# Performance work log

Measured on AMD Instinct MI355X. Metric: run time of the kernel, lower is better.

## Reference

```python
import jax, jax.numpy as jnp
from jax import lax
import numpy as np

K = 31      # avg_pool2d kernel_size
PAD = 15    # avg_pool2d padding
EPS = 1.0
GAMMA = 5.0


def _box_avg(x):
    # Separable 31x31 box filter, stride 1, zero padding 15,
    # count_include_pad=True (PyTorch default) -> always divide by K*K.
    s = lax.reduce_window(x, 0.0, lax.add, (1, 1, K, 1), (1, 1, 1, 1),
                          [(0, 0), (0, 0), (PAD, PAD), (0, 0)])
    s = lax.reduce_window(s, 0.0, lax.add, (1, 1, 1, K), (1, 1, 1, 1),
                          [(0, 0), (0, 0), (0, 0), (PAD, PAD)])
    return s / (K * K)


def setup_inputs() -> dict:
    key = jax.random.key(0)
    k1, k2 = jax.random.split(key)
    shape = (64, 1, 512, 512)  # [B, C, H, W]
    inp = jax.random.uniform(k1, shape, dtype=jnp.float32)
    tgt = jax.random.uniform(k2, shape, dtype=jnp.float32)
    return {"input": inp, "target": tgt}


def reference(input, target):
    weight = 1.0 + GAMMA * jnp.abs(_box_avg(target) - target)
    intersection = jnp.sum(input * target * weight)
    denom = jnp.sum(input * weight) + jnp.sum(target * weight)
    dice = (2.0 * intersection + EPS) / (denom + EPS)
    return 1.0 - dice
```

## Files before the change

kernel.cpp:

```cpp
#include <hip/hip_runtime.h>


#define BATCH 64
#define H     512
#define W     512
#define RBAND 32
#define SLOTS 62
#define NBLK  (BATCH * (H / RBAND))

typedef _Float16 half8 __attribute__((ext_vector_type(8)));

__global__ __launch_bounds__(256, 2) void fused_kernel(const float* __restrict__ tgt,
                                                       const float* __restrict__ inp,
                                                       float4* __restrict__ partials) {
    const int tid  = threadIdx.x;
    const int lane = tid & 63;
    const int wv   = tid >> 6;
    const int g    = blockIdx.x;
    const int blk  = ((g & 7) << 7) | (g >> 3);
    const int band = blk & 15;
    const int b    = blk >> 4;
    const int R0   = band * RBAND;
    const float* timg = tgt + (size_t)b * H * W;
    const float* iimg = inp + (size_t)b * H * W;

    __shared__ __align__(16) unsigned ring[SLOTS * 256];

    const int col0 = lane * 8;
    const int ofs  = lane * 4;

    const float mL1 = (lane >= 1) ? 1.f : 0.f;
    const float mR1 = (lane <= 62) ? 1.f : 0.f;
    const float mL2 = (lane >= 2) ? 1.f : 0.f;
    const float mR2 = (lane <= 61) ? 1.f : 0.f;

    #pragma unroll 2
    for (int k = 0; k < 16; ++k) {
        const int idx = 4 * k + wv;
        if (idx < SLOTS) {
            const int row = R0 - 15 + idx;
            float t[8];
            #pragma unroll
            for (int q = 0; q < 8; ++q) t[q] = 0.f;
            if (row >= 0 && row < H) {
                const float4 v0 = *(const float4*)(timg + (size_t)row * W + col0);
                const float4 v1 = *(const float4*)(timg + (size_t)row * W + col0 + 4);
                t[0] = v0.x; t[1] = v0.y; t[2] = v0.z; t[3] = v0.w;
                t[4] = v1.x; t[5] = v1.y; t[6] = v1.z; t[7] = v1.w;
            }
            const float p1 = t[0];
            const float p2 = p1 + t[1];
            const float p3 = p2 + t[2];
            const float p4 = p3 + t[3];
            const float p5 = p4 + t[4];
            const float p6 = p5 + t[5];
            const float p7 = p6 + t[6];
            const float s  = p7 + t[7];
            const float f1 = s - p1, f2 = s - p2, f3 = s - p3, f4 = s - p4;
            const float f5 = s - p5, f6 = s - p6, f7 = s - p7;

            const float sL1 = __shfl_up(s, 1, 64);
            const float sR1 = __shfl_down(s, 1, 64);
            const float g1 = __shfl_up(f1, 2, 64);
            const float g2 = __shfl_up(f2, 2, 64);
            const float g3 = __shfl_up(f3, 2, 64);
            const float g4 = __shfl_up(f4, 2, 64);
            const float g5 = __shfl_up(f5, 2, 64);
            const float g6 = __shfl_up(f6, 2, 64);
            const float g7 = __shfl_up(f7, 2, 64);
            const float q1 = __shfl_down(p1, 2, 64);
            const float q2 = __shfl_down(p2, 2, 64);
            const float q3 = __shfl_down(p3, 2, 64);
            const float q4 = __shfl_down(p4, 2, 64);
            const float q5 = __shfl_down(p5, 2, 64);
            const float q6 = __shfl_down(p6, 2, 64);
            const float q7 = __shfl_down(p7, 2, 64);

            const float S3 = fmaf(mL1, sL1, fmaf(mR1, sR1, s));
            half8 hv;
            hv[0] = (_Float16)fmaf(mL2, g1, S3);
            hv[1] = (_Float16)fmaf(mL2, g2, fmaf(mR2, q1, S3));
            hv[2] = (_Float16)fmaf(mL2, g3, fmaf(mR2, q2, S3));
            hv[3] = (_Float16)fmaf(mL2, g4, fmaf(mR2, q3, S3));
            hv[4] = (_Float16)fmaf(mL2, g5, fmaf(mR2, q4, S3));
            hv[5] = (_Float16)fmaf(mL2, g6, fmaf(mR2, q5, S3));
            hv[6] = (_Float16)fmaf(mL2, g7, fmaf(mR2, q6, S3));
            hv[7] = (_Float16)fmaf(mR2, q7, S3);
            *(half8*)&ring[idx * 256 + ofs] = hv;
        }
    }
    __syncthreads();

    const int base = 8 * wv;
    float box[8];
    #pragma unroll
    for (int q = 0; q < 8; ++q) box[q] = 0.f;
    #pragma unroll 4
    for (int jj = 0; jj < 31; ++jj) {
        const half8 c = *(const half8*)&ring[(base + jj) * 256 + ofs];
        #pragma unroll
        for (int q = 0; q < 8; ++q) box[q] += (float)c[q];
    }

    const float inv = 1.0f / 961.0f;
    float aI = 0.f, aA = 0.f, aB = 0.f;

    #pragma unroll
    for (int st = 0; st < 8; ++st) {
        const int h = R0 + base + st;

        if (st > 0) {
            const half8 a = *(const half8*)&ring[(base + st + 30) * 256 + ofs];
            const half8 s = *(const half8*)&ring[(base + st - 1) * 256 + ofs];
            #pragma unroll
            for (int q = 0; q < 8; ++q) box[q] += (float)a[q] - (float)s[q];
        }

        const float4 i0 = *(const float4*)(iimg + (size_t)h * W + col0);
        const float4 i1 = *(const float4*)(iimg + (size_t)h * W + col0 + 4);
        const float4 t0 = *(const float4*)(timg + (size_t)h * W + col0);
        const float4 t1 = *(const float4*)(timg + (size_t)h * W + col0 + 4);
        const float tv[8] = {t0.x, t0.y, t0.z, t0.w, t1.x, t1.y, t1.z, t1.w};
        const float iv[8] = {i0.x, i0.y, i0.z, i0.w, i1.x, i1.y, i1.z, i1.w};

        #pragma unroll
        for (int k = 0; k < 8; ++k) {
            const float wgt = fmaf(5.0f, fabsf(fmaf(box[k], inv, -tv[k])), 1.0f);
            const float tw  = tv[k] * wgt;
            aI = fmaf(iv[k], tw, aI);
            aA = fmaf(iv[k], wgt, aA);
            aB += tw;
        }
    }

    #pragma unroll
    for (int off = 32; off > 0; off >>= 1) {
        aI += __shfl_down(aI, off, 64);
        aA += __shfl_down(aA, off, 64);
        aB += __shfl_down(aB, off, 64);
    }
    __syncthreads();
    float* rf = (float*)ring;
    if (lane == 0) { rf[wv] = aI; rf[8 + wv] = aA; rf[16 + wv] = aB; }
    __syncthreads();
    if (tid == 0) {
        float4 o;
        o.x = rf[0] + rf[1] + rf[2] + rf[3];
        o.y = rf[8] + rf[9] + rf[10] + rf[11];
        o.z = rf[16] + rf[17] + rf[18] + rf[19];
        o.w = 0.f;
        partials[g] = o;
    }
}

__global__ __launch_bounds__(1024) void reduce_kernel(const float4* __restrict__ partials,
                                                      float* __restrict__ out) {
    const int tid = threadIdx.x;
    const float4 v = partials[tid];
    float aI = v.x, aA = v.y, aB = v.z;
    #pragma unroll
    for (int off = 32; off > 0; off >>= 1) {
        aI += __shfl_down(aI, off, 64);
        aA += __shfl_down(aA, off, 64);
        aB += __shfl_down(aB, off, 64);
    }
    __shared__ float s[3][16];
    const int wvx = tid >> 6, ln = tid & 63;
    if (ln == 0) { s[0][wvx] = aI; s[1][wvx] = aA; s[2][wvx] = aB; }
    __syncthreads();
    if (tid == 0) {
        float I = 0.f, A = 0.f, Bv = 0.f;
        #pragma unroll
        for (int k = 0; k < 16; ++k) { I += s[0][k]; A += s[1][k]; Bv += s[2][k]; }
        out[0] = 1.0f - (2.0f * I + 1.0f) / (A + Bv + 1.0f);
    }
}

extern "C" void kernel_launch(void* const* d_in, const int* in_sizes, int n_in,
                              void* d_out, int out_size, void* d_ws, size_t ws_size,
                              hipStream_t stream) {
    const float* inp = (const float*)d_in[0];
    const float* tgt = (const float*)d_in[1];
    float* out = (float*)d_out;

    float4* partials = (float4*)d_ws;

    fused_kernel<<<NBLK, 256, 0, stream>>>(tgt, inp, partials);
    reduce_kernel<<<1, 1024, 0, stream>>>(partials, out);
}
```

Baseline: 163.3 us.

## Split fused box filter into global fp16 row-sum pass and sliding column pass

Replaces the single fused kernel, which stored horizontal box sums in an LDS ring per 32-row band, with two kernels. The first writes fp16 horizontal 31-wide sums for every row to a global workspace buffer. The second slides a vertical window down 32-row bands per wave, reading those sums back from global memory, and accumulates the dice terms. This drops the large LDS footprint and the per-band halo recomputation. In exchange it adds a 32 MB fp16 write and read round trip through global memory, plus an extra kernel launch.

```diff
diff --git a/kernel.cpp b/kernel.cpp
--- a/kernel.cpp
+++ b/kernel.cpp
@@ -4,30 +4,21 @@
 #define BATCH 64
 #define H     512
 #define W     512
-#define RBAND 32
-#define SLOTS 62
-#define NBLK  (BATCH * (H / RBAND))
+#define NROWS (BATCH * H)
+#define K1_BLOCKS 2048
+#define K1_WAVES  (K1_BLOCKS * 4)
+#define RB    32
+#define K2_BLOCKS 1024
 
 typedef _Float16 half8 __attribute__((ext_vector_type(8)));
+typedef _Float16 half2v __attribute__((ext_vector_type(2)));
 
-__global__ __launch_bounds__(256, 2) void fused_kernel(const float* __restrict__ tgt,
-                                                       const float* __restrict__ inp,
-                                                       float4* __restrict__ partials) {
+__global__ __launch_bounds__(256) void hrow_kernel(const float* __restrict__ tgt,
+                                                   _Float16* __restrict__ hbuf) {
     const int tid  = threadIdx.x;
     const int lane = tid & 63;
-    const int wv   = tid >> 6;
-    const int g    = blockIdx.x;
-    const int blk  = ((g & 7) << 7) | (g >> 3);
-    const int band = blk & 15;
-    const int b    = blk >> 4;
-    const int R0   = band * RBAND;
-    const float* timg = tgt + (size_t)b * H * W;
-    const float* iimg = inp + (size_t)b * H * W;
-
-    __shared__ __align__(16) unsigned ring[SLOTS * 256];
-
+    const int wid  = blockIdx.x * 4 + (tid >> 6);
     const int col0 = lane * 8;
-    const int ofs  = lane * 4;
 
     const float mL1 = (lane >= 1) ? 1.f : 0.f;
     const float mR1 = (lane <= 62) ? 1.f : 0.f;
@@ -35,102 +26,108 @@
     const float mR2 = (lane <= 61) ? 1.f : 0.f;
 
     #pragma unroll 2
-    for (int k = 0; k < 16; ++k) {
-        const int idx = 4 * k + wv;
-        if (idx < SLOTS) {
-            const int row = R0 - 15 + idx;
-            float t[8];
-            #pragma unroll
-            for (int q = 0; q < 8; ++q) t[q] = 0.f;
-            if (row >= 0 && row < H) {
-                const float4 v0 = *(const float4*)(timg + (size_t)row * W + col0);
-                const float4 v1 = *(const float4*)(timg + (size_t)row * W + col0 + 4);
-                t[0] = v0.x; t[1] = v0.y; t[2] = v0.z; t[3] = v0.w;
-                t[4] = v1.x; t[5] = v1.y; t[6] = v1.z; t[7] = v1.w;
-            }
-            const float p1 = t[0];
-            const float p2 = p1 + t[1];
-            const float p3 = p2 + t[2];
-            const float p4 = p3 + t[3];
-            const float p5 = p4 + t[4];
-            const float p6 = p5 + t[5];
-            const float p7 = p6 + t[6];
-            const float s  = p7 + t[7];
-            const float f1 = s - p1, f2 = s - p2, f3 = s - p3, f4 = s - p4;
-            const float f5 = s - p5, f6 = s - p6, f7 = s - p7;
+    for (int k = 0; k < 4; ++k) {
+        const int r = wid + K1_WAVES * k;
+        const float* trow = tgt + (size_t)r * W;
+        const float4 v0 = *(const float4*)(trow + col0);
+        const float4 v1 = *(const float4*)(trow + col0 + 4);
 
-            const float sL1 = __shfl_up(s, 1, 64);
-            const float sR1 = __shfl_down(s, 1, 64);
-            const float g1 = __shfl_up(f1, 2, 64);
-            const float g2 = __shfl_up(f2, 2, 64);
-            const float g3 = __shfl_up(f3, 2, 64);
-            const float g4 = __shfl_up(f4, 2, 64);
-            const float g5 = __shfl_up(f5, 2, 64);
-            const float g6 = __shfl_up(f6, 2, 64);
-            const float g7 = __shfl_up(f7, 2, 64);
-            const float q1 = __shfl_down(p1, 2, 64);
-            const float q2 = __shfl_down(p2, 2, 64);
-            const float q3 = __shfl_down(p3, 2, 64);
-            const float q4 = __shfl_down(p4, 2, 64);
-            const float q5 = __shfl_down(p5, 2, 64);
-            const float q6 = __shfl_down(p6, 2, 64);
-            const float q7 = __shfl_down(p7, 2, 64);
+        const float p1 = v0.x;
+        const float p2 = p1 + v0.y;
+        const float p3 = p2 + v0.z;
+        const float p4 = p3 + v0.w;
+        const float p5 = p4 + v1.x;
+        const float p6 = p5 + v1.y;
+        const float p7 = p6 + v1.z;
+        const float s  = p7 + v1.w;
+        const float f1 = s - p1, f2 = s - p2, f3 = s - p3, f4 = s - p4;
+        const float f5 = s - p5, f6 = s - p6, f7 = s - p7;
 
-            const float S3 = fmaf(mL1, sL1, fmaf(mR1, sR1, s));
-            half8 hv;
-            hv[0] = (_Float16)fmaf(mL2, g1, S3);
-            hv[1] = (_Float16)fmaf(mL2, g2, fmaf(mR2, q1, S3));
-            hv[2] = (_Float16)fmaf(mL2, g3, fmaf(mR2, q2, S3));
-            hv[3] = (_Float16)fmaf(mL2, g4, fmaf(mR2, q3, S3));
-            hv[4] = (_Float16)fmaf(mL2, g5, fmaf(mR2, q4, S3));
-            hv[5] = (_Float16)fmaf(mL2, g6, fmaf(mR2, q5, S3));
-            hv[6] = (_Float16)fmaf(mL2, g7, fmaf(mR2, q6, S3));
-            hv[7] = (_Float16)fmaf(mR2, q7, S3);
-            *(half8*)&ring[idx * 256 + ofs] = hv;
-        }
+        const float sL1 = __shfl_up(s, 1, 64);
+        const float sR1 = __shfl_down(s, 1, 64);
+        const float g1 = __shfl_up(f1, 2, 64);
+        const float g2 = __shfl_up(f2, 2, 64);
+        const float g3 = __shfl_up(f3, 2, 64);
+        const float g4 = __shfl_up(f4, 2, 64);
+        const float g5 = __shfl_up(f5, 2, 64);
+        const float g6 = __shfl_up(f6, 2, 64);
+        const float g7 = __shfl_up(f7, 2, 64);
+        const float q1 = __shfl_down(p1, 2, 64);
+        const float q2 = __shfl_down(p2, 2, 64);
+        const float q3 = __shfl_down(p3, 2, 64);
+        const float q4 = __shfl_down(p4, 2, 64);
+        const float q5 = __shfl_down(p5, 2, 64);
+        const float q6 = __shfl_down(p6, 2, 64);
+        const float q7 = __shfl_down(p7, 2, 64);
+
+        const float S3 = fmaf(mL1, sL1, fmaf(mR1, sR1, s));
+        half8 hv;
+        hv[0] = (_Float16)fmaf(mL2, g1, S3);
+        hv[1] = (_Float16)fmaf(mL2, g2, fmaf(mR2, q1, S3));
+        hv[2] = (_Float16)fmaf(mL2, g3, fmaf(mR2, q2, S3));
+        hv[3] = (_Float16)fmaf(mL2, g4, fmaf(mR2, q3, S3));
+        hv[4] = (_Float16)fmaf(mL2, g5, fmaf(mR2, q4, S3));
+        hv[5] = (_Float16)fmaf(mL2, g6, fmaf(mR2, q5, S3));
+        hv[6] = (_Float16)fmaf(mL2, g7, fmaf(mR2, q6, S3));
+        hv[7] = (_Float16)fmaf(mR2, q7, S3);
+        *(half8*)(hbuf + (size_t)r * W + col0) = hv;
     }
-    __syncthreads();
+}
 
-    const int base = 8 * wv;
-    float box[8];
-    #pragma unroll
-    for (int q = 0; q < 8; ++q) box[q] = 0.f;
-    #pragma unroll 4
-    for (int jj = 0; jj < 31; ++jj) {
-        const half8 c = *(const half8*)&ring[(base + jj) * 256 + ofs];
-        #pragma unroll
-        for (int q = 0; q < 8; ++q) box[q] += (float)c[q];
+__global__ __launch_bounds__(256) void main_kernel(const float* __restrict__ tgt,
+                                                   const float* __restrict__ inp,
+                                                   const _Float16* __restrict__ hbuf,
+                                                   float4* __restrict__ partials) {
+    const int tid  = threadIdx.x;
+    const int lane = tid & 63;
+    const int wv   = tid >> 6;
+    const int wid  = blockIdx.x * 4 + wv;
+    const int b     = wid >> 6;
+    const int inner = wid & 63;
+    const int cb    = inner & 3;
+    const int band  = inner >> 2;
+    const int r0    = band * RB;
+    const int col   = cb * 128 + lane * 2;
+
+    const float*    timg = tgt  + (size_t)b * H * W;
+    const float*    iimg = inp  + (size_t)b * H * W;
+    const _Float16* himg = hbuf + (size_t)b * H * W;
+
+    float box0 = 0.f, box1 = 0.f;
+    const int j0 = (r0 == 0) ? 15 : 0;
+    #pragma unroll 8
+    for (int j = j0; j < 31; ++j) {
+        const int row = r0 - 15 + j;
+        const half2v hv = *(const half2v*)(himg + (size_t)row * W + col);
+        box0 += (float)hv[0]; box1 += (float)hv[1];
     }
 
     const float inv = 1.0f / 961.0f;
     float aI = 0.f, aA = 0.f, aB = 0.f;
 
-    #pragma unroll
-    for (int st = 0; st < 8; ++st) {
-        const int h = R0 + base + st;
-
+    #pragma unroll 4
+    for (int st = 0; st < RB; ++st) {
+        const int h = r0 + st;
         if (st > 0) {
-            const half8 a = *(const half8*)&ring[(base + st + 30) * 256 + ofs];
-            const half8 s = *(const half8*)&ring[(base + st - 1) * 256 + ofs];
-            #pragma unroll
-            for (int q = 0; q < 8; ++q) box[q] += (float)a[q] - (float)s[q];
+            const int ra = h + 15;
+            const int rs = h - 16;
+            if (ra < H) {
+                const half2v hv = *(const half2v*)(himg + (size_t)ra * W + col);
+                box0 += (float)hv[0]; box1 += (float)hv[1];
+            }
+            if (rs >= 0) {
+                const half2v hv = *(const half2v*)(himg + (size_t)rs * W + col);
+                box0 -= (float)hv[0]; box1 -= (float)hv[1];
+            }
         }
-
-        const float4 i0 = *(const float4*)(iimg + (size_t)h * W + col0);
-        const float4 i1 = *(const float4*)(iimg + (size_t)h * W + col0 + 4);
-        const float4 t0 = *(const float4*)(timg + (size_t)h * W + col0);
-        const float4 t1 = *(const float4*)(timg + (size_t)h * W + col0 + 4);
-        const float tv[8] = {t0.x, t0.y, t0.z, t0.w, t1.x, t1.y, t1.z, t1.w};
-        const float iv[8] = {i0.x, i0.y, i0.z, i0.w, i1.x, i1.y, i1.z, i1.w};
-
-        #pragma unroll
-        for (int k = 0; k < 8; ++k) {
-            const float wgt = fmaf(5.0f, fabsf(fmaf(box[k], inv, -tv[k])), 1.0f);
-            const float tw  = tv[k] * wgt;
-            aI = fmaf(iv[k], tw, aI);
-            aA = fmaf(iv[k], wgt, aA);
-            aB += tw;
-        }
+        const float2 tv = *(const float2*)(timg + (size_t)h * W + col);
+        const float2 iv = *(const float2*)(iimg + (size_t)h * W + col);
+        const float w0 = fmaf(5.0f, fabsf(fmaf(box0, inv, -tv.x)), 1.0f);
+        const float w1 = fmaf(5.0f, fabsf(fmaf(box1, inv, -tv.y)), 1.0f);
+        const float tw0 = tv.x * w0, tw1 = tv.y * w1;
+        aI = fmaf(iv.x, tw0, fmaf(iv.y, tw1, aI));
+        aA = fmaf(iv.x, w0,  fmaf(iv.y, w1,  aA));
+        aB += tw0 + tw1;
     }
 
     #pragma unroll
@@ -139,17 +136,16 @@
         aA += __shfl_down(aA, off, 64);
         aB += __shfl_down(aB, off, 64);
     }
-    __syncthreads();
-    float* rf = (float*)ring;
-    if (lane == 0) { rf[wv] = aI; rf[8 + wv] = aA; rf[16 + wv] = aB; }
+    __shared__ float sm[12];
+    if (lane == 0) { sm[wv] = aI; sm[4 + wv] = aA; sm[8 + wv] = aB; }
     __syncthreads();
     if (tid == 0) {
         float4 o;
-        o.x = rf[0] + rf[1] + rf[2] + rf[3];
-        o.y = rf[8] + rf[9] + rf[10] + rf[11];
-        o.z = rf[16] + rf[17] + rf[18] + rf[19];
+        o.x = sm[0] + sm[1] + sm[2] + sm[3];
+        o.y = sm[4] + sm[5] + sm[6] + sm[7];
+        o.z = sm[8] + sm[9] + sm[10] + sm[11];
         o.w = 0.f;
-        partials[g] = o;
+        partials[blockIdx.x] = o;
     }
 }
 
@@ -183,8 +179,10 @@
     const float* tgt = (const float*)d_in[1];
     float* out = (float*)d_out;
 
-    float4* partials = (float4*)d_ws;
+    _Float16* hbuf = (_Float16*)d_ws;
+    float4* partials = (float4*)((char*)d_ws + (size_t)NROWS * W * sizeof(_Float16));
 
-    fused_kernel<<<NBLK, 256, 0, stream>>>(tgt, inp, partials);
+    hrow_kernel<<<K1_BLOCKS, 256, 0, stream>>>(tgt, hbuf);
+    main_kernel<<<K2_BLOCKS, 256, 0, stream>>>(tgt, inp, hbuf, partials);
     reduce_kernel<<<1, 1024, 0, stream>>>(partials, out);
 }
```

After: 187.0 us. +14.5%, slower.
